# Optimization experiments

Measured on AMD Instinct MI355X. Metric: run time of the kernel, lower is better.

Reference implementation:

```python
import jax, jax.numpy as jnp
import numpy as np

HIDDEN = 512
HEADS = 8
HEAD_DIM = HIDDEN // HEADS
BATCH = 4096
SEQ = 16


def setup_inputs() -> dict:
    key = jax.random.key(0)
    k1, k2, k3 = jax.random.split(key, 3)
    scale = 1.0 / np.sqrt(HIDDEN)
    return {
        "hidden_states": jax.random.normal(k1, (BATCH, SEQ, HIDDEN), dtype=jnp.float32),
        # torch Linear(hidden, 3*hidden, bias=False): weight shape [3*hidden, hidden]
        "w_qkv": jax.random.uniform(k2, (3 * HIDDEN, HIDDEN), dtype=jnp.float32, minval=-scale, maxval=scale),
        "w_o": jax.random.uniform(k3, (HIDDEN, HIDDEN), dtype=jnp.float32, minval=-scale, maxval=scale),
    }


def reference(hidden_states, w_qkv, w_o):
    b, s, _ = hidden_states.shape
    # fused QKV projection: y = x @ W^T
    qkv = jnp.einsum("bsh,oh->bso", hidden_states, w_qkv)
    qkv = qkv.reshape(b, s, 3, HEADS, HEAD_DIM)
    qkv = jnp.transpose(qkv, (2, 0, 3, 1, 4))  # [3, b, heads, s, head_dim]
    q, k, v = qkv[0], qkv[1], qkv[2]
    # scaled dot-product attention (non-causal, dropout=0 in eval)
    scores = jnp.einsum("bhqd,bhkd->bhqk", q, k) / jnp.sqrt(jnp.float32(HEAD_DIM))
    probs = jax.nn.softmax(scores, axis=-1)
    attn = jnp.einsum("bhqk,bhkd->bhqd", probs, v)
    attn = jnp.transpose(attn, (0, 2, 1, 3)).reshape(b, s, HIDDEN)
    return jnp.einsum("bsh,oh->bso", attn, w_o)
```

## Files before the change

### kernel.cpp

```cpp
#include <hip/hip_runtime.h>


#define HID 512

typedef __attribute__((ext_vector_type(4))) float  float4v;
typedef __attribute__((ext_vector_type(8))) short  short8;
typedef __attribute__((ext_vector_type(4))) short  short4v;
typedef __attribute__((ext_vector_type(8))) __bf16 bf16x8;

static __device__ __forceinline__ short bf16rne(float f) {
    union { float f; unsigned u; } v; v.f = f;
    unsigned u = v.u + 0x7FFFu + ((v.u >> 16) & 1u);
    return (short)(u >> 16);
}

static __device__ __forceinline__ short8 pack8(float4v a, float4v b) {
    short8 o;
    o[0] = bf16rne(a[0]); o[1] = bf16rne(a[1]); o[2] = bf16rne(a[2]); o[3] = bf16rne(a[3]);
    o[4] = bf16rne(b[0]); o[5] = bf16rne(b[1]); o[6] = bf16rne(b[2]); o[7] = bf16rne(b[3]);
    return o;
}

static __device__ __forceinline__ void cvt8_store(short* dst, const float* src) {
    float4v a = *(const float4v*)src;
    float4v b = *(const float4v*)(src + 4);
    *(short8*)dst = pack8(a, b);
}

static __device__ __forceinline__ float4v mfma16(short8 a, short8 b, float4v c) {
    union { short8 s; bf16x8 v; } ua, ub;
    ua.s = a; ub.s = b;
    return __builtin_amdgcn_mfma_f32_16x16x32_bf16(ua.v, ub.v, c, 0, 0, 0);
}

static __device__ __forceinline__ void gld16(const short* g, short* l) {
    __builtin_amdgcn_global_load_lds(
        (const __attribute__((address_space(1))) void*)g,
        (__attribute__((address_space(3))) void*)l,
        16, 0, 0);
}

__global__ void cvt_kernel(const float* __restrict__ src, short* __restrict__ dst, int n4) {
    int i = blockIdx.x * 256 + threadIdx.x;
    if (i >= n4) return;
    float4v v = *(const float4v*)(src + (size_t)i * 4);
    short4v o;
    o[0] = bf16rne(v[0]); o[1] = bf16rne(v[1]); o[2] = bf16rne(v[2]); o[3] = bf16rne(v[3]);
    *(short4v*)(dst + (size_t)i * 4) = o;
}

__global__ void repack_wq_kernel(const float* __restrict__ src, short* __restrict__ dst) {
    int i = blockIdx.x * 256 + threadIdx.x;
    int lane = i & 63, t = i >> 6;
    int g = t % 12; t /= 12;
    int ks = t & 1; t >>= 1;
    int kb = t & 7; int h = t >> 3;
    int n = g * 16 + (lane & 15);
    int grow = (n >> 6) * HID + h * 64 + (n & 63);
    int col = kb * 64 + ks * 32 + (lane >> 4) * 8;
    cvt8_store(&dst[(size_t)i * 8], &src[(size_t)grow * HID + col]);
}

__global__ void repack_wo_kernel(const float* __restrict__ src, short* __restrict__ dst) {
    int i = blockIdx.x * 256 + threadIdx.x;
    int lane = i & 63, t = i >> 6;
    int gg = t & 7; t >>= 3;
    int ks = t & 1; t >>= 1;
    int kb = t & 7; int nt = t >> 3;
    int row = nt * 128 + gg * 16 + (lane & 15);
    int col = kb * 64 + ks * 32 + (lane >> 4) * 8;
    cvt8_store(&dst[(size_t)i * 8], &src[(size_t)row * HID + col]);
}

__global__ __launch_bounds__(512, 4)
void qkv_head_kernel(const float* __restrict__ x, const short* __restrict__ xb, const int use_xb,
                     const float* __restrict__ wqf, const short* __restrict__ wqb, const int use_wb,
                     short* __restrict__ attnb, float* __restrict__ attnf, const int use_ab) {
    __shared__ __align__(16) union {
        struct { short a[2][128 * 64]; } st;
        struct { short q[128 * 72]; short k[128 * 72]; short vt[64 * 152]; short p[8 * 16 * 40]; } at;
    } L;

    const int tid  = threadIdx.x;
    const int wave = tid >> 6;
    const int lane = tid & 63;
    const int ln   = lane & 15;
    const int q8   = (lane >> 4) * 8;
    const int qrow = (lane >> 4) * 4;
    const int wr   = wave >> 2;
    const int wc   = wave & 3;

    const int g   = blockIdx.x;
    const int xcd = g & 7;
    const int j   = g >> 3;
    const int h   = j & 7;
    const int mt  = (j >> 3) * 8 + xcd;
    const int m0  = mt * 128;

    float4v acc[4][3];
    #pragma unroll
    for (int fr = 0; fr < 4; ++fr)
        #pragma unroll
        for (int fc = 0; fc < 3; ++fc)
            acc[fr][fc] = (float4v){0.f, 0.f, 0.f, 0.f};

    auto stageA = [&](int buf, int kb) {
        if (use_xb) {
            #pragma unroll
            for (int i = 0; i < 2; ++i) {
                const int cg  = i * 512 + tid;
                const int row = cg >> 3;
                const int c8  = ((cg & 7) ^ (row & 7)) * 8;
                gld16(&xb[(size_t)(m0 + row) * HID + kb * 64 + c8],
                      &L.st.a[buf][(i * 512 + (wave << 6)) * 8]);
            }
        } else {
            #pragma unroll
            for (int i = 0; i < 2; ++i) {
                const int cg  = i * 512 + tid;
                const int row = cg >> 3;
                const int c8  = ((cg & 7) ^ (row & 7)) * 8;
                cvt8_store(&L.st.a[buf][cg * 8], &x[(size_t)(m0 + row) * HID + kb * 64 + c8]);
            }
        }
    };
    auto loadKs = [&](short8* d, int kb, int ks) {
        if (use_wb) {
            #pragma unroll
            for (int fc = 0; fc < 3; ++fc) {
                const int chunk = ((h * 8 + kb) * 2 + ks) * 12 + wc * 3 + fc;
                d[fc] = *(const short8*)&wqb[(size_t)chunk * 512 + lane * 8];
            }
        } else {
            #pragma unroll
            for (int fc = 0; fc < 3; ++fc) {
                const int n    = (wc * 3 + fc) * 16 + ln;
                const int grow = (n >> 6) * HID + h * 64 + (n & 63);
                const float* s = &wqf[(size_t)grow * HID + kb * 64 + ks * 32 + q8];
                d[fc] = pack8(*(const float4v*)s, *(const float4v*)(s + 4));
            }
        }
    };

    short8 bf[3][3];
    loadKs(bf[0], 0, 0);
    loadKs(bf[1], 0, 1);
    stageA(0, 0);
    __syncthreads();

    #pragma unroll
    for (int kb = 0; kb < 8; ++kb) {
        const int cur = kb & 1;
        const int s0 = (2 * kb) % 3, s1 = (2 * kb + 1) % 3, sf = (2 * kb + 2) % 3;
        if (kb < 7) {
            stageA(cur ^ 1, kb + 1);
            loadKs(bf[sf], kb + 1, 0);
        }
        {
            const int cslot = (lane >> 4);
            short8 a[4];
            #pragma unroll
            for (int fr = 0; fr < 4; ++fr) {
                const int row = wr * 64 + fr * 16 + ln;
                a[fr] = *(const short8*)&L.st.a[cur][row * 64 + ((cslot ^ (row & 7)) << 3)];
            }
            #pragma unroll
            for (int fr = 0; fr < 4; ++fr)
                #pragma unroll
                for (int fc = 0; fc < 3; ++fc)
                    acc[fr][fc] = mfma16(a[fr], bf[s0][fc], acc[fr][fc]);
        }
        if (kb < 7) loadKs(bf[s0], kb + 1, 1);
        {
            const int cslot = 4 + (lane >> 4);
            short8 a[4];
            #pragma unroll
            for (int fr = 0; fr < 4; ++fr) {
                const int row = wr * 64 + fr * 16 + ln;
                a[fr] = *(const short8*)&L.st.a[cur][row * 64 + ((cslot ^ (row & 7)) << 3)];
            }
            #pragma unroll
            for (int fr = 0; fr < 4; ++fr)
                #pragma unroll
                for (int fc = 0; fc < 3; ++fc)
                    acc[fr][fc] = mfma16(a[fr], bf[s1][fc], acc[fr][fc]);
        }
        __syncthreads();
    }

    #pragma unroll
    for (int fr = 0; fr < 4; ++fr) {
        #pragma unroll
        for (int fc = 0; fc < 3; ++fc) {
            const int nb = wc * 48 + fc * 16;
            const int n  = nb + ln;
            const int mb = wr * 64 + fr * 16 + qrow;
            const float4v v = acc[fr][fc];
            if (nb < 64) {
                #pragma unroll
                for (int r = 0; r < 4; ++r)
                    L.at.q[(mb + r) * 72 + n] = bf16rne(v[r] * 0.125f);
            } else if (nb < 128) {
                #pragma unroll
                for (int r = 0; r < 4; ++r)
                    L.at.k[(mb + r) * 72 + (n - 64)] = bf16rne(v[r]);
            } else {
                #pragma unroll
                for (int r = 0; r < 4; ++r)
                    L.at.vt[(n - 128) * 152 + mb + r] = bf16rne(v[r]);
            }
        }
    }
    for (int i = tid; i < 64 * 24; i += 512)
        L.at.vt[(i / 24) * 152 + 128 + (i % 24)] = 0;
    for (int i = tid; i < 8 * 16 * 16; i += 512)
        L.at.p[(i >> 8) * 640 + ((i >> 4) & 15) * 40 + 16 + (i & 15)] = 0;
    __syncthreads();

    {
        const int rb = wave * 16;
        const short* qp = &L.at.q[(rb + ln) * 72 + q8];
        const short* kp = &L.at.k[(rb + ln) * 72 + q8];
        short8 aq0 = *(const short8*)qp;
        short8 aq1 = *(const short8*)(qp + 32);
        short8 bk0 = *(const short8*)kp;
        short8 bk1 = *(const short8*)(kp + 32);
        float4v s = (float4v){0.f, 0.f, 0.f, 0.f};
        s = mfma16(aq0, bk0, s);
        s = mfma16(aq1, bk1, s);

        float4v mx = s;
        #pragma unroll
        for (int off = 1; off < 16; off <<= 1)
            #pragma unroll
            for (int r = 0; r < 4; ++r)
                mx[r] = fmaxf(mx[r], __shfl_xor(mx[r], off));
        float4v p;
        #pragma unroll
        for (int r = 0; r < 4; ++r) p[r] = __expf(s[r] - mx[r]);
        float4v sm = p;
        #pragma unroll
        for (int off = 1; off < 16; off <<= 1)
            #pragma unroll
            for (int r = 0; r < 4; ++r)
                sm[r] += __shfl_xor(sm[r], off);
        #pragma unroll
        for (int r = 0; r < 4; ++r)
            L.at.p[wave * 640 + (qrow + r) * 40 + ln] = bf16rne(p[r] * __builtin_amdgcn_rcpf(sm[r]));

        short8 ap = *(const short8*)&L.at.p[wave * 640 + ln * 40 + q8];
        #pragma unroll
        for (int dc = 0; dc < 4; ++dc) {
            short8 bv = *(const short8*)&L.at.vt[(dc * 16 + ln) * 152 + rb + q8];
            float4v o = (float4v){0.f, 0.f, 0.f, 0.f};
            o = mfma16(ap, bv, o);
            #pragma unroll
            for (int r = 0; r < 4; ++r) {
                const size_t oi = (size_t)(m0 + rb + qrow + r) * HID + h * 64 + dc * 16 + ln;
                if (use_ab) attnb[oi] = bf16rne(o[r]);
                else        attnf[oi] = o[r];
            }
        }
    }
}

__global__ __launch_bounds__(256, 3)
void oproj_kernel(const short* __restrict__ attnb, const short* __restrict__ wob,
                  float* __restrict__ out) {
    __shared__ __align__(16) short A[2][128 * 64];

    const int tid  = threadIdx.x;
    const int wave = tid >> 6;
    const int lane = tid & 63;
    const int ln   = lane & 15;
    const int qrow = (lane >> 4) * 4;
    const int wr   = wave >> 1;
    const int wc   = wave & 1;

    const int g   = blockIdx.x;
    const int xcd = g & 7;
    const int j   = g >> 3;
    const int nt  = j & 3;
    const int mt  = (j >> 2) * 8 + xcd;
    const int m0  = mt * 128;
    const int n0  = nt * 128;

    float4v acc[4][4];
    #pragma unroll
    for (int fr = 0; fr < 4; ++fr)
        #pragma unroll
        for (int fc = 0; fc < 4; ++fc)
            acc[fr][fc] = (float4v){0.f, 0.f, 0.f, 0.f};

    auto stageA = [&](int buf, int kb) {
        #pragma unroll
        for (int i = 0; i < 4; ++i) {
            const int cg  = i * 256 + tid;
            const int row = cg >> 3;
            const int c8  = ((cg & 7) ^ (row & 7)) * 8;
            gld16(&attnb[(size_t)(m0 + row) * HID + kb * 64 + c8],
                  &A[buf][(i * 256 + (wave << 6)) * 8]);
        }
    };
    auto loadKs = [&](short8* d, int kb, int ks) {
        #pragma unroll
        for (int fc = 0; fc < 4; ++fc) {
            const int chunk = ((nt * 8 + kb) * 2 + ks) * 8 + wc * 4 + fc;
            d[fc] = *(const short8*)&wob[(size_t)chunk * 512 + lane * 8];
        }
    };

    short8 bf[3][4];
    loadKs(bf[0], 0, 0);
    loadKs(bf[1], 0, 1);
    stageA(0, 0);
    __syncthreads();

    #pragma unroll
    for (int kb = 0; kb < 8; ++kb) {
        const int cur = kb & 1;
        const int s0 = (2 * kb) % 3, s1 = (2 * kb + 1) % 3, sf = (2 * kb + 2) % 3;
        if (kb < 7) {
            stageA(cur ^ 1, kb + 1);
            loadKs(bf[sf], kb + 1, 0);
        }
        {
            const int cslot = (lane >> 4);
            short8 a[4];
            #pragma unroll
            for (int fr = 0; fr < 4; ++fr) {
                const int row = wr * 64 + fr * 16 + ln;
                a[fr] = *(const short8*)&A[cur][row * 64 + ((cslot ^ (row & 7)) << 3)];
            }
            #pragma unroll
            for (int fr = 0; fr < 4; ++fr)
                #pragma unroll
                for (int fc = 0; fc < 4; ++fc)
                    acc[fr][fc] = mfma16(a[fr], bf[s0][fc], acc[fr][fc]);
        }
        if (kb < 7) loadKs(bf[s0], kb + 1, 1);
        {
            const int cslot = 4 + (lane >> 4);
            short8 a[4];
            #pragma unroll
            for (int fr = 0; fr < 4; ++fr) {
                const int row = wr * 64 + fr * 16 + ln;
                a[fr] = *(const short8*)&A[cur][row * 64 + ((cslot ^ (row & 7)) << 3)];
            }
            #pragma unroll
            for (int fr = 0; fr < 4; ++fr)
                #pragma unroll
                for (int fc = 0; fc < 4; ++fc)
                    acc[fr][fc] = mfma16(a[fr], bf[s1][fc], acc[fr][fc]);
        }
        __syncthreads();
    }

    #pragma unroll
    for (int fr = 0; fr < 4; ++fr)
        #pragma unroll
        for (int fc = 0; fc < 4; ++fc)
            #pragma unroll
            for (int r = 0; r < 4; ++r)
                out[(size_t)(m0 + wr * 64 + fr * 16 + qrow + r) * HID +
                    n0 + wc * 64 + fc * 16 + ln] = acc[fr][fc][r];
}

__global__ __launch_bounds__(512, 2)
void oproj_inplace_kernel(float* __restrict__ io, const float* __restrict__ wof,
                          const short* __restrict__ wob, const int use_wb) {
    __shared__ __align__(16) short sA[64 * 40];
    __shared__ __align__(16) short sW2[512 * 40];

    const int tid  = threadIdx.x;
    const int wave = tid >> 6;
    const int lane = tid & 63;
    const int ln   = lane & 15;
    const int q8   = (lane >> 4) * 8;
    const int qrow = (lane >> 4) * 4;
    const int m0   = blockIdx.x * 64;

    float4v acc[4][4];
    #pragma unroll
    for (int fr = 0; fr < 4; ++fr)
        #pragma unroll
        for (int fc = 0; fc < 4; ++fc)
            acc[fr][fc] = (float4v){0.f, 0.f, 0.f, 0.f};

    for (int kb = 0; kb < 16; ++kb) {
        __syncthreads();
        if (tid < 256) {
            int row = tid >> 2, c8 = (tid & 3) * 8;
            cvt8_store(&sA[row * 40 + c8], &io[(size_t)(m0 + row) * HID + kb * 32 + c8]);
        }
        #pragma unroll
        for (int it = 0; it < 4; ++it) {
            int gg = tid + it * 512;
            int n = gg >> 2, c8 = (gg & 3) * 8;
            if (use_wb)
                *(short8*)&sW2[n * 40 + c8] = *(const short8*)&wob[(size_t)n * HID + kb * 32 + c8];
            else
                cvt8_store(&sW2[n * 40 + c8], &wof[(size_t)n * HID + kb * 32 + c8]);
        }
        __syncthreads();
        short8 a[4], b[4];
        #pragma unroll
        for (int fr = 0; fr < 4; ++fr)
            a[fr] = *(const short8*)&sA[(fr * 16 + ln) * 40 + q8];
        #pragma unroll
        for (int fc = 0; fc < 4; ++fc)
            b[fc] = *(const short8*)&sW2[(wave * 64 + fc * 16 + ln) * 40 + q8];
        #pragma unroll
        for (int fr = 0; fr < 4; ++fr)
            #pragma unroll
            for (int fc = 0; fc < 4; ++fc)
                acc[fr][fc] = mfma16(a[fr], b[fc], acc[fr][fc]);
    }
    #pragma unroll
    for (int fr = 0; fr < 4; ++fr)
        #pragma unroll
        for (int fc = 0; fc < 4; ++fc)
            #pragma unroll
            for (int r = 0; r < 4; ++r)
                io[(size_t)(m0 + fr * 16 + qrow + r) * HID + wave * 64 + fc * 16 + ln] =
                    acc[fr][fc][r];
}

extern "C" void kernel_launch(void* const* d_in, const int* in_sizes, int n_in,
                              void* d_out, int out_size, void* d_ws, size_t ws_size,
                              hipStream_t stream) {
    const float* x    = (const float*)d_in[0];
    const float* wqkv = (const float*)d_in[1];
    const float* wo   = (const float*)d_in[2];
    float* out = (float*)d_out;

    const size_t n_x  = (size_t)65536 * HID;
    const size_t n_wq = (size_t)1536 * HID;
    const size_t n_wo = (size_t)HID * HID;
    const size_t szA = (n_x * 2 + n_wq + n_wo) * 2;
    const size_t szB = (n_x + n_wq + n_wo) * 2;
    const size_t szC = (n_wq + n_wo) * 2;

    short* xb = nullptr; short* attnb = nullptr; short* wqb = nullptr; short* wob = nullptr;
    int use_xb = 0, use_ab = 0, use_wb = 0;
    short* ws = (short*)d_ws;

    if (d_ws && ws_size >= szA) {
        use_xb = use_ab = use_wb = 1;
        xb = ws; attnb = xb + n_x; wqb = attnb + n_x; wob = wqb + n_wq;
    } else if (d_ws && ws_size >= szB) {
        use_ab = use_wb = 1;
        attnb = ws; wqb = attnb + n_x; wob = wqb + n_wq;
    } else if (d_ws && ws_size >= szC) {
        use_wb = 1;
        wqb = ws; wob = wqb + n_wq;
    }

    if (use_xb)
        cvt_kernel<<<(int)(n_x / 1024), 256, 0, stream>>>(x, xb, (int)(n_x / 4));
    if (use_wb) {
        repack_wq_kernel<<<384, 256, 0, stream>>>(wqkv, wqb);
        if (use_ab)
            repack_wo_kernel<<<128, 256, 0, stream>>>(wo, wob);
        else
            cvt_kernel<<<(int)(n_wo / 1024), 256, 0, stream>>>(wo, wob, (int)(n_wo / 4));
    }

    qkv_head_kernel<<<4096, 512, 0, stream>>>(x, xb, use_xb, wqkv, wqb, use_wb,
                                              attnb, out , use_ab);

    if (use_ab)
        oproj_kernel<<<2048, 256, 0, stream>>>(attnb, wob, out);
    else
        oproj_inplace_kernel<<<1024, 512, 0, stream>>>(out, wo, wob, use_wb);
}
```

Before: 408.9 us.

## Stage QKV weights through LDS, merge prep kernels, deepen oproj B prefetch

Merges the x conversion, QKV weight conversion and W_o repack into one prep kernel, which removes separate launches. W_qkv is now converted in plain row-major order rather than fragment order. The QKV projection kernel now loads its weight tile into a double-buffered, swizzled LDS buffer with async global-to-LDS loads, replacing per-wave register fragment loads, and its k-loop is no longer forced to unroll. The output projection prefetches both k-halves of the next B block up front using four register buffers. The costs are a larger LDS footprint in the QKV kernel, which may reduce occupancy, and more live registers in oproj.

Measured after the change: 372.8 us. 1.1x faster.

```diff
diff --git a/kernel.cpp b/kernel.cpp
--- a/kernel.cpp
+++ b/kernel.cpp
@@ -27,6 +27,13 @@
     *(short8*)dst = pack8(a, b);
 }
 
+static __device__ __forceinline__ void cvt4_store(short* dst, const float* src) {
+    float4v v = *(const float4v*)src;
+    short4v o;
+    o[0] = bf16rne(v[0]); o[1] = bf16rne(v[1]); o[2] = bf16rne(v[2]); o[3] = bf16rne(v[3]);
+    *(short4v*)dst = o;
+}
+
 static __device__ __forceinline__ float4v mfma16(short8 a, short8 b, float4v c) {
     union { short8 s; bf16x8 v; } ua, ub;
     ua.s = a; ub.s = b;
@@ -40,36 +47,30 @@
         16, 0, 0);
 }
 
-__global__ void cvt_kernel(const float* __restrict__ src, short* __restrict__ dst, int n4) {
-    int i = blockIdx.x * 256 + threadIdx.x;
-    if (i >= n4) return;
-    float4v v = *(const float4v*)(src + (size_t)i * 4);
-    short4v o;
-    o[0] = bf16rne(v[0]); o[1] = bf16rne(v[1]); o[2] = bf16rne(v[2]); o[3] = bf16rne(v[3]);
-    *(short4v*)(dst + (size_t)i * 4) = o;
-}
-
-__global__ void repack_wq_kernel(const float* __restrict__ src, short* __restrict__ dst) {
-    int i = blockIdx.x * 256 + threadIdx.x;
-    int lane = i & 63, t = i >> 6;
-    int g = t % 12; t /= 12;
-    int ks = t & 1; t >>= 1;
-    int kb = t & 7; int h = t >> 3;
-    int n = g * 16 + (lane & 15);
-    int grow = (n >> 6) * HID + h * 64 + (n & 63);
-    int col = kb * 64 + ks * 32 + (lane >> 4) * 8;
-    cvt8_store(&dst[(size_t)i * 8], &src[(size_t)grow * HID + col]);
-}
-
-__global__ void repack_wo_kernel(const float* __restrict__ src, short* __restrict__ dst) {
-    int i = blockIdx.x * 256 + threadIdx.x;
-    int lane = i & 63, t = i >> 6;
-    int gg = t & 7; t >>= 3;
-    int ks = t & 1; t >>= 1;
-    int kb = t & 7; int nt = t >> 3;
-    int row = nt * 128 + gg * 16 + (lane & 15);
-    int col = kb * 64 + ks * 32 + (lane >> 4) * 8;
-    cvt8_store(&dst[(size_t)i * 8], &src[(size_t)row * HID + col]);
+__global__ void prep_kernel(const float* __restrict__ x, short* __restrict__ xb,
+                            const float* __restrict__ wqkv, short* __restrict__ wqb,
+                            const float* __restrict__ wo, short* __restrict__ wob,
+                            const int wo_frag, const int b_wq, const int b_wo) {
+    const int blk = blockIdx.x, tid = threadIdx.x;
+    if (blk < b_wq) {
+        const size_t i = (size_t)blk * 256 + tid;
+        cvt4_store(&xb[i * 4], &x[i * 4]);
+    } else if (blk < b_wo) {
+        const size_t i = (size_t)(blk - b_wq) * 256 + tid;
+        cvt4_store(&wqb[i * 4], &wqkv[i * 4]);
+    } else if (wo_frag) {
+        const int i = (blk - b_wo) * 256 + tid;
+        const int lane = i & 63; int t = i >> 6;
+        const int gg = t & 7; t >>= 3;
+        const int ks = t & 1; t >>= 1;
+        const int kb = t & 7; const int nt = t >> 3;
+        const int row = nt * 128 + gg * 16 + (lane & 15);
+        const int col = kb * 64 + ks * 32 + (lane >> 4) * 8;
+        cvt8_store(&wob[(size_t)i * 8], &wo[(size_t)row * HID + col]);
+    } else {
+        const size_t i = (size_t)(blk - b_wo) * 256 + tid;
+        cvt4_store(&wob[i * 4], &wo[i * 4]);
+    }
 }
 
 __global__ __launch_bounds__(512, 4)
@@ -77,7 +78,7 @@
                      const float* __restrict__ wqf, const short* __restrict__ wqb, const int use_wb,
                      short* __restrict__ attnb, float* __restrict__ attnf, const int use_ab) {
     __shared__ __align__(16) union {
-        struct { short a[2][128 * 64]; } st;
+        struct { short a[2][128 * 64]; short b[2][192 * 64]; } st;
         struct { short q[128 * 72]; short k[128 * 72]; short vt[64 * 152]; short p[8 * 16 * 40]; } at;
     } L;
 
@@ -124,68 +125,61 @@
             }
         }
     };
-    auto loadKs = [&](short8* d, int kb, int ks) {
+    auto stageB = [&](int buf, int kb) {
         if (use_wb) {
             #pragma unroll
-            for (int fc = 0; fc < 3; ++fc) {
-                const int chunk = ((h * 8 + kb) * 2 + ks) * 12 + wc * 3 + fc;
-                d[fc] = *(const short8*)&wqb[(size_t)chunk * 512 + lane * 8];
+            for (int i = 0; i < 3; ++i) {
+                const int cg   = i * 512 + tid;
+                const int n    = cg >> 3;
+                const int c8   = ((cg & 7) ^ (n & 7)) * 8;
+                const int grow = (n >> 6) * HID + h * 64 + (n & 63);
+                gld16(&wqb[(size_t)grow * HID + kb * 64 + c8],
+                      &L.st.b[buf][(i * 512 + (wave << 6)) * 8]);
             }
         } else {
             #pragma unroll
-            for (int fc = 0; fc < 3; ++fc) {
-                const int n    = (wc * 3 + fc) * 16 + ln;
+            for (int i = 0; i < 3; ++i) {
+                const int cg   = i * 512 + tid;
+                const int n    = cg >> 3;
+                const int c8   = ((cg & 7) ^ (n & 7)) * 8;
                 const int grow = (n >> 6) * HID + h * 64 + (n & 63);
-                const float* s = &wqf[(size_t)grow * HID + kb * 64 + ks * 32 + q8];
-                d[fc] = pack8(*(const float4v*)s, *(const float4v*)(s + 4));
+                cvt8_store(&L.st.b[buf][cg * 8], &wqf[(size_t)grow * HID + kb * 64 + c8]);
             }
         }
     };
 
-    short8 bf[3][3];
-    loadKs(bf[0], 0, 0);
-    loadKs(bf[1], 0, 1);
     stageA(0, 0);
+    stageB(0, 0);
     __syncthreads();
 
-    #pragma unroll
+    int cur = 0;
     for (int kb = 0; kb < 8; ++kb) {
-        const int cur = kb & 1;
-        const int s0 = (2 * kb) % 3, s1 = (2 * kb + 1) % 3, sf = (2 * kb + 2) % 3;
         if (kb < 7) {
             stageA(cur ^ 1, kb + 1);
-            loadKs(bf[sf], kb + 1, 0);
-        }
-        {
-            const int cslot = (lane >> 4);
-            short8 a[4];
+            stageB(cur ^ 1, kb + 1);
+        }
+        #pragma unroll
+        for (int ks = 0; ks < 2; ++ks) {
+            const int cslot = ks * 4 + (lane >> 4);
+            short8 a[4], b[3];
             #pragma unroll
             for (int fr = 0; fr < 4; ++fr) {
                 const int row = wr * 64 + fr * 16 + ln;
                 a[fr] = *(const short8*)&L.st.a[cur][row * 64 + ((cslot ^ (row & 7)) << 3)];
             }
             #pragma unroll
+            for (int fc = 0; fc < 3; ++fc) {
+                const int row = wc * 48 + fc * 16 + ln;
+                b[fc] = *(const short8*)&L.st.b[cur][row * 64 + ((cslot ^ (row & 7)) << 3)];
+            }
+            #pragma unroll
             for (int fr = 0; fr < 4; ++fr)
                 #pragma unroll
                 for (int fc = 0; fc < 3; ++fc)
-                    acc[fr][fc] = mfma16(a[fr], bf[s0][fc], acc[fr][fc]);
-        }
-        if (kb < 7) loadKs(bf[s0], kb + 1, 1);
-        {
-            const int cslot = 4 + (lane >> 4);
-            short8 a[4];
-            #pragma unroll
-            for (int fr = 0; fr < 4; ++fr) {
-                const int row = wr * 64 + fr * 16 + ln;
-                a[fr] = *(const short8*)&L.st.a[cur][row * 64 + ((cslot ^ (row & 7)) << 3)];
-            }
-            #pragma unroll
-            for (int fr = 0; fr < 4; ++fr)
-                #pragma unroll
-                for (int fc = 0; fc < 3; ++fc)
-                    acc[fr][fc] = mfma16(a[fr], bf[s1][fc], acc[fr][fc]);
+                    acc[fr][fc] = mfma16(a[fr], b[fc], acc[fr][fc]);
         }
         __syncthreads();
+        cur ^= 1;
     }
 
     #pragma unroll
@@ -310,7 +304,7 @@
         }
     };
 
-    short8 bf[3][4];
+    short8 bf[4][4];
     loadKs(bf[0], 0, 0);
     loadKs(bf[1], 0, 1);
     stageA(0, 0);
@@ -319,10 +313,12 @@
     #pragma unroll
     for (int kb = 0; kb < 8; ++kb) {
         const int cur = kb & 1;
-        const int s0 = (2 * kb) % 3, s1 = (2 * kb + 1) % 3, sf = (2 * kb + 2) % 3;
+        const int s0 = (2 * kb) & 3, s1 = (2 * kb + 1) & 3;
+        const int t0 = (2 * kb + 2) & 3, t1 = (2 * kb + 3) & 3;
         if (kb < 7) {
             stageA(cur ^ 1, kb + 1);
-            loadKs(bf[sf], kb + 1, 0);
+            loadKs(bf[t0], kb + 1, 0);
+            loadKs(bf[t1], kb + 1, 1);
         }
         {
             const int cslot = (lane >> 4);
@@ -338,7 +334,6 @@
                 for (int fc = 0; fc < 4; ++fc)
                     acc[fr][fc] = mfma16(a[fr], bf[s0][fc], acc[fr][fc]);
         }
-        if (kb < 7) loadKs(bf[s0], kb + 1, 1);
         {
             const int cslot = 4 + (lane >> 4);
             short8 a[4];
@@ -456,14 +451,14 @@
         wqb = ws; wob = wqb + n_wq;
     }
 
-    if (use_xb)
-        cvt_kernel<<<(int)(n_x / 1024), 256, 0, stream>>>(x, xb, (int)(n_x / 4));
     if (use_wb) {
-        repack_wq_kernel<<<384, 256, 0, stream>>>(wqkv, wqb);
-        if (use_ab)
-            repack_wo_kernel<<<128, 256, 0, stream>>>(wo, wob);
-        else
-            cvt_kernel<<<(int)(n_wo / 1024), 256, 0, stream>>>(wo, wob, (int)(n_wo / 4));
+        const int nbx = use_xb ? 32768 : 0;
+        const int b_wq = nbx;
+        const int b_wo = nbx + 768;
+        const int wo_frag = use_ab ? 1 : 0;
+        const int grid = b_wo + (wo_frag ? 128 : 256);
+        prep_kernel<<<grid, 256, 0, stream>>>(x, xb, wqkv, wqb, wo, wob,
+                                              wo_frag, b_wq, b_wo);
     }
 
     qkv_head_kernel<<<4096, 512, 0, stream>>>(x, xb, use_xb, wqkv, wqb, use_wb,
```
